# Performance work log

Hardware: AMD Instinct MI355X
Metric: run time of the kernel (lower is better)

Reference implementation:

```python
import jax, jax.numpy as jnp
import numpy as np

N = 100000        # nodes
E = 3200000       # edges (avg degree 32)
D_IN, D_H, D_OUT = 128, 128, 64
EPS = 1e-5        # BatchNorm eps


def setup_inputs() -> dict:
    key = jax.random.key(0)
    ks = jax.random.split(key, 12)
    s = 0.1
    return {
        "x": jax.random.normal(ks[0], (N, D_IN), jnp.float32),
        "edge_index": jax.random.randint(ks[1], (2, E), 0, N, jnp.int32),
        "W1": jax.random.normal(ks[2], (D_IN, D_H), jnp.float32) * s,
        "b1": jnp.zeros((D_H,), jnp.float32),
        "W2": jax.random.normal(ks[3], (D_H, D_H), jnp.float32) * s,
        "b2": jnp.zeros((D_H,), jnp.float32),
        "W3": jax.random.normal(ks[4], (D_H, D_OUT), jnp.float32) * s,
        "b3": jnp.zeros((D_OUT,), jnp.float32),
        "g1": jnp.ones((D_H,), jnp.float32),
        "be1": jnp.zeros((D_H,), jnp.float32),
        "g2": jnp.ones((D_H,), jnp.float32),
        "be2": jnp.zeros((D_H,), jnp.float32),
    }


def reference(x, edge_index, W1, b1, W2, b2, W3, b3, g1, be1, g2, be2):
    # GCNConv normalization: add self-loops, symmetric deg^-1/2 A deg^-1/2
    loop = jnp.arange(N, dtype=edge_index.dtype)
    src = jnp.concatenate([edge_index[0], loop])   # [E+N]
    dst = jnp.concatenate([edge_index[1], loop])   # [E+N]
    deg = jax.ops.segment_sum(jnp.ones(src.shape, x.dtype), dst, num_segments=N)
    dinv = jnp.where(deg > 0, jax.lax.rsqrt(deg), 0.0)
    norm = (dinv[src] * dinv[dst])[:, None]        # [E+N, 1]

    def conv(h, W, b):
        h = h @ W                                   # dense transform [N, d]
        msg = h[src] * norm                         # gather + scale [E+N, d]
        return jax.ops.segment_sum(msg, dst, num_segments=N) + b

    def bn(h, g, be):  # BatchNorm1d over nodes (batch stats, eval-style dropout)
        m = h.mean(axis=0)
        v = h.var(axis=0)
        return (h - m) * jax.lax.rsqrt(v + EPS) * g + be

    h = jax.nn.relu(bn(conv(x, W1, b1), g1, be1))
    h = jax.nn.relu(bn(conv(h, W2, b2), g2, be2))
    h = conv(h, W3, b3)
    return jax.nn.softmax(h, axis=1)
```

## Files before the change

### kernel.cpp

```cpp
#include <hip/hip_runtime.h>
#include <hip/hip_fp16.h>

constexpr int   NN   = 100000;
constexpr int   NE   = 3200000;
constexpr float BN_EPS = 1e-5f;

constexpr int MG_B  = (NN / 32 + 3) / 4;
constexpr int CNT_B = NE / 256;
constexpr int SC_B  = NN * 128 / 4 / 256;

typedef _Float16 half8 __attribute__((ext_vector_type(8)));
typedef float    floatx16 __attribute__((ext_vector_type(16)));

__global__ __launch_bounds__(256) void k_wprep_all(const float* __restrict__ W1,
                                                   const float* __restrict__ W2,
                                                   const float* __restrict__ W3,
                                                   _Float16* __restrict__ Wt1,
                                                   _Float16* __restrict__ Wt2,
                                                   _Float16* __restrict__ Wt3) {
  int idx = blockIdx.x * 256 + threadIdx.x;
  if (idx < 16384) {
    int k = idx >> 7, n = idx & 127;
    Wt1[n * 128 + k] = (_Float16)W1[idx];
  } else if (idx < 32768) {
    int j = idx - 16384, k = j >> 7, n = j & 127;
    Wt2[n * 128 + k] = (_Float16)W2[j];
  } else if (idx < 40960) {
    int j = idx - 32768, k = j >> 6, n = j & 63;
    Wt3[n * 128 + k] = (_Float16)W3[j];
  }
}

__global__ __launch_bounds__(256) void k_f1(const int* __restrict__ dst,
                                            int* __restrict__ deg,
                                            int* __restrict__ slot,
                                            const float* __restrict__ x,
                                            const _Float16* __restrict__ Wt1,
                                            _Float16* __restrict__ C) {
  if (blockIdx.x < MG_B) {
    int wid  = (blockIdx.x * 256 + threadIdx.x) >> 6;
    int lane = threadIdx.x & 63;
    if (wid >= NN / 32) return;
    const int m = lane & 31;
    const int q = lane >> 5;
    const int row0 = wid * 32;
    const float* Arow = x + (size_t)(row0 + m) * 128 + q * 8;

    floatx16 acc[4] = {};
#pragma unroll
    for (int s = 0; s < 8; ++s) {
      float4 a0 = *(const float4*)(Arow + 16 * s);
      float4 a1 = *(const float4*)(Arow + 16 * s + 4);
      half8 af;
      af[0] = (_Float16)a0.x; af[1] = (_Float16)a0.y;
      af[2] = (_Float16)a0.z; af[3] = (_Float16)a0.w;
      af[4] = (_Float16)a1.x; af[5] = (_Float16)a1.y;
      af[6] = (_Float16)a1.z; af[7] = (_Float16)a1.w;
#pragma unroll
      for (int ct = 0; ct < 4; ++ct) {
        half8 bf = *(const half8*)(Wt1 + (size_t)(ct * 32 + m) * 128 + q * 8 + 16 * s);
        acc[ct] = __builtin_amdgcn_mfma_f32_32x32x16_f16(af, bf, acc[ct], 0, 0, 0);
      }
    }
#pragma unroll
    for (int ct = 0; ct < 4; ++ct)
#pragma unroll
      for (int r = 0; r < 16; ++r) {
        int row = (r & 3) + 8 * (r >> 2) + 4 * q;
        C[(size_t)(row0 + row) * 128 + ct * 32 + m] = (_Float16)acc[ct][r];
      }
  } else {
    int e = (blockIdx.x - MG_B) * 256 + threadIdx.x;
    if (e < NE) slot[e] = atomicAdd(&deg[dst[e]], 1);
  }
}

__global__ __launch_bounds__(256) void k_scan_a(const int* __restrict__ deg,
                                                float* __restrict__ dinv,
                                                int* __restrict__ rowptr,
                                                int* __restrict__ bsum) {
  __shared__ int sd[256];
  int t = threadIdx.x;
  int i = blockIdx.x * 256 + t;
  int v = (i < NN) ? deg[i] : 0;
  if (i < NN) dinv[i] = rsqrtf((float)(v + 1));
  sd[t] = v;
  __syncthreads();
  for (int off = 1; off < 256; off <<= 1) {
    int x = (t >= off) ? sd[t - off] : 0;
    __syncthreads();
    sd[t] += x;
    __syncthreads();
  }
  if (i < NN) rowptr[i] = sd[t] - v;
  if (t == 255) bsum[blockIdx.x] = sd[255];
}

__global__ __launch_bounds__(512) void k_scan_b(int* __restrict__ bsum, int nb) {
  __shared__ int sd[512];
  int t = threadIdx.x;
  int v = (t < nb) ? bsum[t] : 0;
  sd[t] = v;
  __syncthreads();
  for (int off = 1; off < 512; off <<= 1) {
    int x = (t >= off) ? sd[t - off] : 0;
    __syncthreads();
    sd[t] += x;
    __syncthreads();
  }
  if (t < nb) bsum[t] = sd[t] - v;
}

__global__ __launch_bounds__(256) void k_scan_c(int* __restrict__ rowptr,
                                                const int* __restrict__ bsum) {
  int i = blockIdx.x * 256 + threadIdx.x;
  if (i < NN) rowptr[i] += bsum[blockIdx.x];
  if (i == 0) rowptr[NN] = NE;
}

__global__ __launch_bounds__(256) void k_f2(const int* __restrict__ ei,
                                            const int* __restrict__ rowptr,
                                            const int* __restrict__ slot,
                                            int* __restrict__ csrc,
                                            const float* __restrict__ dinv,
                                            uint2* __restrict__ Hf) {
  if (blockIdx.x < SC_B) {
    int i = blockIdx.x * 256 + threadIdx.x;
    int row = i >> 5;
    float dv = dinv[row];
    uint2 v = Hf[i];
    __half2 h0 = *(__half2*)&v.x;
    __half2 h1 = *(__half2*)&v.y;
    float2 f0 = __half22float2(h0);
    float2 f1 = __half22float2(h1);
    h0 = __floats2half2_rn(f0.x * dv, f0.y * dv);
    h1 = __floats2half2_rn(f1.x * dv, f1.y * dv);
    v.x = *(unsigned*)&h0;
    v.y = *(unsigned*)&h1;
    Hf[i] = v;
  } else {
    int e = (blockIdx.x - SC_B) * 256 + threadIdx.x;
    if (e >= NE) return;
    int s = ei[e];
    int d = ei[NE + e];
    csrc[rowptr[d] + slot[e]] = s;
  }
}

template <int BN_>
__global__ __launch_bounds__(256) void k_mgemm(const _Float16* __restrict__ A,
                                               const _Float16* __restrict__ Wt,
                                               const float* __restrict__ scale,
                                               const float* __restrict__ shift,
                                               const float* __restrict__ dinv,
                                               _Float16* __restrict__ C) {
  constexpr int NCT = BN_ / 32;
  int wid  = (blockIdx.x * 256 + threadIdx.x) >> 6;
  int lane = threadIdx.x & 63;
  if (wid >= NN / 32) return;
  const int m = lane & 31;
  const int q = lane >> 5;
  const int row0 = wid * 32;

  const _Float16* Arow = A + (size_t)(row0 + m) * 128 + q * 8;

  floatx16 acc[NCT] = {};

#pragma unroll
  for (int s = 0; s < 8; ++s) {
    half8 raw = *(const half8*)(Arow + 16 * s);
    int k0 = 16 * s + q * 8;
    half8 af;
#pragma unroll
    for (int j = 0; j < 8; ++j) {
      float a = fmaxf(fmaf((float)raw[j], scale[k0 + j], shift[k0 + j]), 0.f);
      af[j] = (_Float16)a;
    }
#pragma unroll
    for (int ct = 0; ct < NCT; ++ct) {
      half8 bf = *(const half8*)(Wt + (size_t)(ct * 32 + m) * 128 + q * 8 + 16 * s);
      acc[ct] = __builtin_amdgcn_mfma_f32_32x32x16_f16(af, bf, acc[ct], 0, 0, 0);
    }
  }

#pragma unroll
  for (int ct = 0; ct < NCT; ++ct)
#pragma unroll
    for (int r = 0; r < 16; ++r) {
      int row = (r & 3) + 8 * (r >> 2) + 4 * q;
      float dv = dinv[row0 + row];
      C[(size_t)(row0 + row) * BN_ + ct * 32 + m] = (_Float16)(acc[ct][r] * dv);
    }
}

__global__ __launch_bounds__(256) void k_agg128(const __half* __restrict__ H,
                                                const float* __restrict__ dinv,
                                                const int* __restrict__ rowptr,
                                                const int* __restrict__ srcs,
                                                __half2* __restrict__ out) {
  int wid  = (blockIdx.x * 256 + threadIdx.x) >> 6;
  int lane = threadIdx.x & 63;
  if (wid >= NN) return;
  const __half2* Hp = (const __half2*)H;
  float2 acc = __half22float2(Hp[(size_t)wid * 64 + lane]);
  int beg = rowptr[wid], end = rowptr[wid + 1];
  int e = beg;
  int end8 = beg + ((end - beg) & ~7);
  for (; e < end8; e += 8) {
    __half2 v0 = Hp[(size_t)srcs[e+0] * 64 + lane];
    __half2 v1 = Hp[(size_t)srcs[e+1] * 64 + lane];
    __half2 v2 = Hp[(size_t)srcs[e+2] * 64 + lane];
    __half2 v3 = Hp[(size_t)srcs[e+3] * 64 + lane];
    __half2 v4 = Hp[(size_t)srcs[e+4] * 64 + lane];
    __half2 v5 = Hp[(size_t)srcs[e+5] * 64 + lane];
    __half2 v6 = Hp[(size_t)srcs[e+6] * 64 + lane];
    __half2 v7 = Hp[(size_t)srcs[e+7] * 64 + lane];
    float2 f0 = __half22float2(v0), f1 = __half22float2(v1);
    float2 f2 = __half22float2(v2), f3 = __half22float2(v3);
    float2 f4 = __half22float2(v4), f5 = __half22float2(v5);
    float2 f6 = __half22float2(v6), f7 = __half22float2(v7);
    acc.x += (f0.x + f1.x) + (f2.x + f3.x) + (f4.x + f5.x) + (f6.x + f7.x);
    acc.y += (f0.y + f1.y) + (f2.y + f3.y) + (f4.y + f5.y) + (f6.y + f7.y);
  }
  for (; e < end; ++e) {
    float2 f = __half22float2(Hp[(size_t)srcs[e] * 64 + lane]);
    acc.x += f.x; acc.y += f.y;
  }
  float di = dinv[wid];
  out[(size_t)wid * 64 + lane] = __floats2half2_rn(acc.x * di, acc.y * di);
}

__global__ __launch_bounds__(256) void k_agg64_softmax(const __half* __restrict__ H,
                                                       const float* __restrict__ dinv,
                                                       const int* __restrict__ rowptr,
                                                       const int* __restrict__ srcs,
                                                       const float* __restrict__ b3,
                                                       float* __restrict__ out) {
  int wid  = (blockIdx.x * 256 + threadIdx.x) >> 6;
  int lane = threadIdx.x & 63;
  if (wid >= NN) return;
  float acc = __half2float(H[(size_t)wid * 64 + lane]);
  int beg = rowptr[wid], end = rowptr[wid + 1];
  int e = beg;
  int end8 = beg + ((end - beg) & ~7);
  for (; e < end8; e += 8) {
    float v0 = __half2float(H[(size_t)srcs[e+0] * 64 + lane]);
    float v1 = __half2float(H[(size_t)srcs[e+1] * 64 + lane]);
    float v2 = __half2float(H[(size_t)srcs[e+2] * 64 + lane]);
    float v3 = __half2float(H[(size_t)srcs[e+3] * 64 + lane]);
    float v4 = __half2float(H[(size_t)srcs[e+4] * 64 + lane]);
    float v5 = __half2float(H[(size_t)srcs[e+5] * 64 + lane]);
    float v6 = __half2float(H[(size_t)srcs[e+6] * 64 + lane]);
    float v7 = __half2float(H[(size_t)srcs[e+7] * 64 + lane]);
    acc += (v0 + v1) + (v2 + v3) + (v4 + v5) + (v6 + v7);
  }
  for (; e < end; ++e)
    acc += __half2float(H[(size_t)srcs[e] * 64 + lane]);
  acc = acc * dinv[wid] + b3[lane];

  float m = acc;
#pragma unroll
  for (int off = 32; off > 0; off >>= 1) m = fmaxf(m, __shfl_xor(m, off));
  float ev = __expf(acc - m);
  float s = ev;
#pragma unroll
  for (int off = 32; off > 0; off >>= 1) s += __shfl_xor(s, off);
  out[(size_t)wid * 64 + lane] = ev / s;
}

__global__ __launch_bounds__(256) void k_stats(const __half2* __restrict__ H2,
                                               float* __restrict__ S1,
                                               float* __restrict__ S2) {
  int t = threadIdx.x;
  int p = t & 63;
  int r = t >> 6;
  float2 s1 = {0.f, 0.f}, s2 = {0.f, 0.f};
  for (int row = blockIdx.x * 4 + r; row < NN; row += gridDim.x * 4) {
    float2 v = __half22float2(H2[(size_t)row * 64 + p]);
    s1.x += v.x; s1.y += v.y;
    s2.x += v.x * v.x; s2.y += v.y * v.y;
  }
  __shared__ float2 l1[256], l2[256];
  l1[t] = s1; l2[t] = s2;
  __syncthreads();
  if (t < 128) {
    l1[t].x += l1[t+128].x; l1[t].y += l1[t+128].y;
    l2[t].x += l2[t+128].x; l2[t].y += l2[t+128].y;
  }
  __syncthreads();
  if (t < 64) {
    float2 a1 = l1[t], b1 = l1[t+64];
    float2 a2 = l2[t], b2 = l2[t+64];
    atomicAdd(&S1[2*p+0], a1.x + b1.x);
    atomicAdd(&S1[2*p+1], a1.y + b1.y);
    atomicAdd(&S2[2*p+0], a2.x + b2.x);
    atomicAdd(&S2[2*p+1], a2.y + b2.y);
  }
}

__global__ void k_finalize(const float* __restrict__ S1, const float* __restrict__ S2,
                           const float* __restrict__ g,  const float* __restrict__ be,
                           float* __restrict__ scale,    float* __restrict__ shift) {
  int t = threadIdx.x;
  float mean = S1[t] * (1.0f / NN);
  float var  = S2[t] * (1.0f / NN) - mean * mean;
  float is   = rsqrtf(var + BN_EPS);
  float sc   = g[t] * is;
  scale[t] = sc;
  shift[t] = be[t] - mean * sc;
}

extern "C" void kernel_launch(void* const* d_in, const int* in_sizes, int n_in,
                              void* d_out, int out_size, void* d_ws, size_t ws_size,
                              hipStream_t stream) {
  (void)in_sizes; (void)n_in; (void)out_size; (void)ws_size;
  const float* x   = (const float*)d_in[0];
  const int*   ei  = (const int*)d_in[1];
  const float* W1  = (const float*)d_in[2];
  const float* W2  = (const float*)d_in[4];
  const float* W3  = (const float*)d_in[6];
  const float* b3  = (const float*)d_in[7];
  const float* g1  = (const float*)d_in[8];
  const float* be1 = (const float*)d_in[9];
  const float* g2  = (const float*)d_in[10];
  const float* be2 = (const float*)d_in[11];
  float* out = (float*)d_out;

  char* ws = (char*)d_ws;
  size_t off = 0;
  auto take = [&](size_t bytes) -> char* {
    char* p = ws + off;
    off = (off + bytes + 255) & ~(size_t)255;
    return p;
  };
  int*   deg    = (int*)  take((size_t)NN * 4);
  float* S1a    = (float*)take(128 * 4);
  float* S2a    = (float*)take(128 * 4);
  float* S1b    = (float*)take(128 * 4);
  float* S2b    = (float*)take(128 * 4);
  size_t zero_bytes = off;
  float* scale1 = (float*)take(128 * 4);
  float* shift1 = (float*)take(128 * 4);
  float* scale2 = (float*)take(128 * 4);
  float* shift2 = (float*)take(128 * 4);
  float* dinv   = (float*)take((size_t)NN * 4);
  int*   rowptr = (int*)  take((size_t)(NN + 1) * 4);
  int*   bsum   = (int*)  take(1024 * 4);
  int*   slot   = (int*)  take((size_t)NE * 4);
  int*   csrc   = (int*)  take((size_t)NE * 4);
  _Float16* Wt1 = (_Float16*)take((size_t)128 * 128 * 2);
  _Float16* Wt2 = (_Float16*)take((size_t)128 * 128 * 2);
  _Float16* Wt3 = (_Float16*)take((size_t)64 * 128 * 2);
  _Float16* Hf  = (_Float16*)take((size_t)NN * 128 * 2);
  _Float16* hB  = (_Float16*)take((size_t)NN * 128 * 2);

  (void)hipMemsetAsync(d_ws, 0, zero_bytes, stream);

  const int nbN  = (NN + 255) / 256;
  const int mgB  = MG_B;
  const int aggB = (NN + 3) / 4;

  k_wprep_all<<<160, 256, 0, stream>>>(W1, W2, W3, Wt1, Wt2, Wt3);

  k_f1<<<MG_B + CNT_B, 256, 0, stream>>>(ei + NE, deg, slot, x, Wt1, Hf);

  k_scan_a<<<nbN, 256, 0, stream>>>(deg, dinv, rowptr, bsum);
  k_scan_b<<<1, 512, 0, stream>>>(bsum, nbN);
  k_scan_c<<<nbN, 256, 0, stream>>>(rowptr, bsum);

  k_f2<<<SC_B + CNT_B, 256, 0, stream>>>(ei, rowptr, slot, csrc, dinv, (uint2*)Hf);

  k_agg128<<<aggB, 256, 0, stream>>>((const __half*)Hf, dinv, rowptr, csrc, (__half2*)hB);
  k_stats<<<1024, 256, 0, stream>>>((const __half2*)hB, S1a, S2a);
  k_finalize<<<1, 128, 0, stream>>>(S1a, S2a, g1, be1, scale1, shift1);

  k_mgemm<128><<<mgB, 256, 0, stream>>>(hB, Wt2, scale1, shift1, dinv, Hf);
  k_agg128<<<aggB, 256, 0, stream>>>((const __half*)Hf, dinv, rowptr, csrc, (__half2*)hB);
  k_stats<<<1024, 256, 0, stream>>>((const __half2*)hB, S1b, S2b);
  k_finalize<<<1, 128, 0, stream>>>(S1b, S2b, g2, be2, scale2, shift2);

  k_mgemm<64><<<mgB, 256, 0, stream>>>(hB, Wt3, scale2, shift2, dinv, Hf);
  k_agg64_softmax<<<aggB, 256, 0, stream>>>((const __half*)Hf, dinv, rowptr, csrc, b3, out);
}
```

Baseline: 840.5 us.

## Build CSR via two-level bucket sort instead of global atomic degree counting

Replaces the global-atomic degree count plus slot-based scatter with a two-level counting sort. Per-chunk shared-memory histograms over 128-node buckets are scanned, edges are scattered into buckets, then each bucket is locally sorted by node to produce rowptr, dinv and csrc. This removes contended global atomics and the random csrc writes. The separate pre-scaling of the first-layer features by dinv is dropped; the first aggregation instead applies source-node dinv inline, which adds per-edge dinv gathers to that pass. Node ids are packed into 17 bits and the local offset into the upper bits, which holds for N=100000.

```diff
diff --git a/kernel.cpp b/kernel.cpp
--- a/kernel.cpp
+++ b/kernel.cpp
@@ -6,8 +6,9 @@
 constexpr float BN_EPS = 1e-5f;
 
 constexpr int MG_B  = (NN / 32 + 3) / 4;
-constexpr int CNT_B = NE / 256;
-constexpr int SC_B  = NN * 128 / 4 / 256;
+constexpr int NB    = (NN + 127) / 128;
+constexpr int HB    = 256;
+constexpr int CHUNK = NE / HB;
 
 typedef _Float16 half8 __attribute__((ext_vector_type(8)));
 typedef float    floatx16 __attribute__((ext_vector_type(16)));
@@ -32,11 +33,11 @@
 }
 
 __global__ __launch_bounds__(256) void k_f1(const int* __restrict__ dst,
-                                            int* __restrict__ deg,
-                                            int* __restrict__ slot,
+                                            int* __restrict__ blkhist,
                                             const float* __restrict__ x,
                                             const _Float16* __restrict__ Wt1,
                                             _Float16* __restrict__ C) {
+  __shared__ int h[NB];
   if (blockIdx.x < MG_B) {
     int wid  = (blockIdx.x * 256 + threadIdx.x) >> 6;
     int lane = threadIdx.x & 63;
@@ -70,80 +71,121 @@
         C[(size_t)(row0 + row) * 128 + ct * 32 + m] = (_Float16)acc[ct][r];
       }
   } else {
-    int e = (blockIdx.x - MG_B) * 256 + threadIdx.x;
-    if (e < NE) slot[e] = atomicAdd(&deg[dst[e]], 1);
-  }
-}
-
-__global__ __launch_bounds__(256) void k_scan_a(const int* __restrict__ deg,
-                                                float* __restrict__ dinv,
-                                                int* __restrict__ rowptr,
-                                                int* __restrict__ bsum) {
-  __shared__ int sd[256];
+    int j = blockIdx.x - MG_B;
+    int t = threadIdx.x;
+    for (int b = t; b < NB; b += 256) h[b] = 0;
+    __syncthreads();
+    int base = j * CHUNK;
+    for (int e = base + t; e < base + CHUNK; e += 256)
+      atomicAdd(&h[dst[e] >> 7], 1);
+    __syncthreads();
+    for (int b = t; b < NB; b += 256) blkhist[j * NB + b] = h[b];
+  }
+}
+
+__global__ __launch_bounds__(256) void k_scan_bkt_a(const int* __restrict__ blkhist,
+                                                    int* __restrict__ blkbase,
+                                                    int* __restrict__ total) {
+  int wid  = (blockIdx.x * 256 + threadIdx.x) >> 6;
+  int lane = threadIdx.x & 63;
+  if (wid >= NB) return;
+  int i0 = lane * 4;
+  int v0 = blkhist[(i0 + 0) * NB + wid];
+  int v1 = blkhist[(i0 + 1) * NB + wid];
+  int v2 = blkhist[(i0 + 2) * NB + wid];
+  int v3 = blkhist[(i0 + 3) * NB + wid];
+  int lt = v0 + v1 + v2 + v3;
+  int inc = lt;
+#pragma unroll
+  for (int off = 1; off < 64; off <<= 1) {
+    int xx = __shfl_up(inc, off);
+    if (lane >= off) inc += xx;
+  }
+  int exc = inc - lt;
+  blkbase[(i0 + 0) * NB + wid] = exc;
+  blkbase[(i0 + 1) * NB + wid] = exc + v0;
+  blkbase[(i0 + 2) * NB + wid] = exc + v0 + v1;
+  blkbase[(i0 + 3) * NB + wid] = exc + v0 + v1 + v2;
+  if (lane == 63) total[wid] = inc;
+}
+
+__global__ __launch_bounds__(1024) void k_scan_bkt_b(const int* __restrict__ total,
+                                                     int* __restrict__ bbase) {
+  __shared__ int s[1024];
   int t = threadIdx.x;
-  int i = blockIdx.x * 256 + t;
-  int v = (i < NN) ? deg[i] : 0;
-  if (i < NN) dinv[i] = rsqrtf((float)(v + 1));
-  sd[t] = v;
-  __syncthreads();
-  for (int off = 1; off < 256; off <<= 1) {
-    int x = (t >= off) ? sd[t - off] : 0;
-    __syncthreads();
-    sd[t] += x;
-    __syncthreads();
-  }
-  if (i < NN) rowptr[i] = sd[t] - v;
-  if (t == 255) bsum[blockIdx.x] = sd[255];
-}
-
-__global__ __launch_bounds__(512) void k_scan_b(int* __restrict__ bsum, int nb) {
-  __shared__ int sd[512];
+  int v = (t < NB) ? total[t] : 0;
+  s[t] = v;
+  __syncthreads();
+  for (int off = 1; off < 1024; off <<= 1) {
+    int xx = (t >= off) ? s[t - off] : 0;
+    __syncthreads();
+    s[t] += xx;
+    __syncthreads();
+  }
+  if (t < NB) bbase[t] = s[t] - v;
+  if (t == NB - 1) bbase[NB] = s[t];
+}
+
+__global__ __launch_bounds__(256) void k_scatter(const int* __restrict__ ei,
+                                                 const int* __restrict__ bbase,
+                                                 const int* __restrict__ blkbase,
+                                                 int* __restrict__ ebuf) {
+  __shared__ int cur[NB];
+  int i = blockIdx.x;
   int t = threadIdx.x;
-  int v = (t < nb) ? bsum[t] : 0;
-  sd[t] = v;
-  __syncthreads();
-  for (int off = 1; off < 512; off <<= 1) {
-    int x = (t >= off) ? sd[t - off] : 0;
-    __syncthreads();
-    sd[t] += x;
-    __syncthreads();
-  }
-  if (t < nb) bsum[t] = sd[t] - v;
-}
-
-__global__ __launch_bounds__(256) void k_scan_c(int* __restrict__ rowptr,
-                                                const int* __restrict__ bsum) {
-  int i = blockIdx.x * 256 + threadIdx.x;
-  if (i < NN) rowptr[i] += bsum[blockIdx.x];
-  if (i == 0) rowptr[NN] = NE;
-}
-
-__global__ __launch_bounds__(256) void k_f2(const int* __restrict__ ei,
-                                            const int* __restrict__ rowptr,
-                                            const int* __restrict__ slot,
-                                            int* __restrict__ csrc,
-                                            const float* __restrict__ dinv,
-                                            uint2* __restrict__ Hf) {
-  if (blockIdx.x < SC_B) {
-    int i = blockIdx.x * 256 + threadIdx.x;
-    int row = i >> 5;
-    float dv = dinv[row];
-    uint2 v = Hf[i];
-    __half2 h0 = *(__half2*)&v.x;
-    __half2 h1 = *(__half2*)&v.y;
-    float2 f0 = __half22float2(h0);
-    float2 f1 = __half22float2(h1);
-    h0 = __floats2half2_rn(f0.x * dv, f0.y * dv);
-    h1 = __floats2half2_rn(f1.x * dv, f1.y * dv);
-    v.x = *(unsigned*)&h0;
-    v.y = *(unsigned*)&h1;
-    Hf[i] = v;
-  } else {
-    int e = (blockIdx.x - SC_B) * 256 + threadIdx.x;
-    if (e >= NE) return;
+  for (int b = t; b < NB; b += 256) cur[b] = bbase[b] + blkbase[i * NB + b];
+  __syncthreads();
+  int base = i * CHUNK;
+  for (int e = base + t; e < base + CHUNK; e += 256) {
     int s = ei[e];
     int d = ei[NE + e];
-    csrc[rowptr[d] + slot[e]] = s;
+    int b = d >> 7;
+    int pos = atomicAdd(&cur[b], 1);
+    ebuf[pos] = s | ((d & 127) << 17);
+  }
+}
+
+__global__ __launch_bounds__(256) void k_bucket(const int* __restrict__ bbase,
+                                                const int* __restrict__ ebuf,
+                                                int* __restrict__ rowptr,
+                                                float* __restrict__ dinv,
+                                                int* __restrict__ csrc) {
+  __shared__ int degL[128];
+  __shared__ int sc[128];
+  __shared__ int curL[128];
+  int b = blockIdx.x;
+  int t = threadIdx.x;
+  int e0 = bbase[b], e1 = bbase[b + 1];
+  if (t < 128) degL[t] = 0;
+  __syncthreads();
+  for (int e = e0 + t; e < e1; e += 256)
+    atomicAdd(&degL[ebuf[e] >> 17], 1);
+  __syncthreads();
+  if (t < 128) sc[t] = degL[t];
+  __syncthreads();
+  for (int off = 1; off < 128; off <<= 1) {
+    int xx = 0;
+    if (t < 128 && t >= off) xx = sc[t - off];
+    __syncthreads();
+    if (t < 128) sc[t] += xx;
+    __syncthreads();
+  }
+  if (t < 128) {
+    int node = b * 128 + t;
+    if (node < NN) {
+      int d = degL[t];
+      int exc = sc[t] - d;
+      rowptr[node] = e0 + exc;
+      dinv[node] = rsqrtf((float)(d + 1));
+      curL[t] = exc;
+    }
+  }
+  if (b == NB - 1 && t == 0) rowptr[NN] = NE;
+  __syncthreads();
+  for (int e = e0 + t; e < e1; e += 256) {
+    int p = ebuf[e];
+    int pos = atomicAdd(&curL[p >> 17], 1);
+    csrc[e0 + pos] = p & 0x1FFFF;
   }
 }
 
@@ -193,6 +235,7 @@
     }
 }
 
+template <bool SRCSCALE>
 __global__ __launch_bounds__(256) void k_agg128(const __half* __restrict__ H,
                                                 const float* __restrict__ dinv,
                                                 const int* __restrict__ rowptr,
@@ -202,31 +245,55 @@
   int lane = threadIdx.x & 63;
   if (wid >= NN) return;
   const __half2* Hp = (const __half2*)H;
-  float2 acc = __half22float2(Hp[(size_t)wid * 64 + lane]);
+  float di = dinv[wid];
+  float2 self = __half22float2(Hp[(size_t)wid * 64 + lane]);
+  float2 acc;
+  if (SRCSCALE) { acc.x = self.x * di; acc.y = self.y * di; }
+  else          { acc = self; }
   int beg = rowptr[wid], end = rowptr[wid + 1];
   int e = beg;
   int end8 = beg + ((end - beg) & ~7);
   for (; e < end8; e += 8) {
-    __half2 v0 = Hp[(size_t)srcs[e+0] * 64 + lane];
-    __half2 v1 = Hp[(size_t)srcs[e+1] * 64 + lane];
-    __half2 v2 = Hp[(size_t)srcs[e+2] * 64 + lane];
-    __half2 v3 = Hp[(size_t)srcs[e+3] * 64 + lane];
-    __half2 v4 = Hp[(size_t)srcs[e+4] * 64 + lane];
-    __half2 v5 = Hp[(size_t)srcs[e+5] * 64 + lane];
-    __half2 v6 = Hp[(size_t)srcs[e+6] * 64 + lane];
-    __half2 v7 = Hp[(size_t)srcs[e+7] * 64 + lane];
+    int s0 = srcs[e+0], s1 = srcs[e+1], s2 = srcs[e+2], s3 = srcs[e+3];
+    int s4 = srcs[e+4], s5 = srcs[e+5], s6 = srcs[e+6], s7 = srcs[e+7];
+    __half2 v0 = Hp[(size_t)s0 * 64 + lane];
+    __half2 v1 = Hp[(size_t)s1 * 64 + lane];
+    __half2 v2 = Hp[(size_t)s2 * 64 + lane];
+    __half2 v3 = Hp[(size_t)s3 * 64 + lane];
+    __half2 v4 = Hp[(size_t)s4 * 64 + lane];
+    __half2 v5 = Hp[(size_t)s5 * 64 + lane];
+    __half2 v6 = Hp[(size_t)s6 * 64 + lane];
+    __half2 v7 = Hp[(size_t)s7 * 64 + lane];
     float2 f0 = __half22float2(v0), f1 = __half22float2(v1);
     float2 f2 = __half22float2(v2), f3 = __half22float2(v3);
     float2 f4 = __half22float2(v4), f5 = __half22float2(v5);
     float2 f6 = __half22float2(v6), f7 = __half22float2(v7);
-    acc.x += (f0.x + f1.x) + (f2.x + f3.x) + (f4.x + f5.x) + (f6.x + f7.x);
-    acc.y += (f0.y + f1.y) + (f2.y + f3.y) + (f4.y + f5.y) + (f6.y + f7.y);
+    if (SRCSCALE) {
+      float d0 = dinv[s0], d1 = dinv[s1], d2 = dinv[s2], d3 = dinv[s3];
+      float d4 = dinv[s4], d5 = dinv[s5], d6 = dinv[s6], d7 = dinv[s7];
+      acc.x = fmaf(f0.x, d0, acc.x); acc.y = fmaf(f0.y, d0, acc.y);
+      acc.x = fmaf(f1.x, d1, acc.x); acc.y = fmaf(f1.y, d1, acc.y);
+      acc.x = fmaf(f2.x, d2, acc.x); acc.y = fmaf(f2.y, d2, acc.y);
+      acc.x = fmaf(f3.x, d3, acc.x); acc.y = fmaf(f3.y, d3, acc.y);
+      acc.x = fmaf(f4.x, d4, acc.x); acc.y = fmaf(f4.y, d4, acc.y);
+      acc.x = fmaf(f5.x, d5, acc.x); acc.y = fmaf(f5.y, d5, acc.y);
+      acc.x = fmaf(f6.x, d6, acc.x); acc.y = fmaf(f6.y, d6, acc.y);
+      acc.x = fmaf(f7.x, d7, acc.x); acc.y = fmaf(f7.y, d7, acc.y);
+    } else {
+      acc.x += (f0.x + f1.x) + (f2.x + f3.x) + (f4.x + f5.x) + (f6.x + f7.x);
+      acc.y += (f0.y + f1.y) + (f2.y + f3.y) + (f4.y + f5.y) + (f6.y + f7.y);
+    }
   }
   for (; e < end; ++e) {
-    float2 f = __half22float2(Hp[(size_t)srcs[e] * 64 + lane]);
-    acc.x += f.x; acc.y += f.y;
-  }
-  float di = dinv[wid];
+    int s = srcs[e];
+    float2 f = __half22float2(Hp[(size_t)s * 64 + lane]);
+    if (SRCSCALE) {
+      float dd = dinv[s];
+      acc.x = fmaf(f.x, dd, acc.x); acc.y = fmaf(f.y, dd, acc.y);
+    } else {
+      acc.x += f.x; acc.y += f.y;
+    }
+  }
   out[(size_t)wid * 64 + lane] = __floats2half2_rn(acc.x * di, acc.y * di);
 }
 
@@ -333,7 +400,6 @@
     off = (off + bytes + 255) & ~(size_t)255;
     return p;
   };
-  int*   deg    = (int*)  take((size_t)NN * 4);
   float* S1a    = (float*)take(128 * 4);
   float* S2a    = (float*)take(128 * 4);
   float* S1b    = (float*)take(128 * 4);
@@ -345,8 +411,11 @@
   float* shift2 = (float*)take(128 * 4);
   float* dinv   = (float*)take((size_t)NN * 4);
   int*   rowptr = (int*)  take((size_t)(NN + 1) * 4);
-  int*   bsum   = (int*)  take(1024 * 4);
-  int*   slot   = (int*)  take((size_t)NE * 4);
+  int*   bbase  = (int*)  take((size_t)(NB + 1) * 4);
+  int*   total  = (int*)  take((size_t)NB * 4);
+  int*   blkhist= (int*)  take((size_t)HB * NB * 4);
+  int*   blkbase= (int*)  take((size_t)HB * NB * 4);
+  int*   ebuf   = (int*)  take((size_t)NE * 4);
   int*   csrc   = (int*)  take((size_t)NE * 4);
   _Float16* Wt1 = (_Float16*)take((size_t)128 * 128 * 2);
   _Float16* Wt2 = (_Float16*)take((size_t)128 * 128 * 2);
@@ -356,26 +425,25 @@
 
   (void)hipMemsetAsync(d_ws, 0, zero_bytes, stream);
 
-  const int nbN  = (NN + 255) / 256;
   const int mgB  = MG_B;
   const int aggB = (NN + 3) / 4;
+  const int scanAB = (NB + 3) / 4;
 
   k_wprep_all<<<160, 256, 0, stream>>>(W1, W2, W3, Wt1, Wt2, Wt3);
 
-  k_f1<<<MG_B + CNT_B, 256, 0, stream>>>(ei + NE, deg, slot, x, Wt1, Hf);
-
-  k_scan_a<<<nbN, 256, 0, stream>>>(deg, dinv, rowptr, bsum);
-  k_scan_b<<<1, 512, 0, stream>>>(bsum, nbN);
-  k_scan_c<<<nbN, 256, 0, stream>>>(rowptr, bsum);
-
-  k_f2<<<SC_B + CNT_B, 256, 0, stream>>>(ei, rowptr, slot, csrc, dinv, (uint2*)Hf);
-
-  k_agg128<<<aggB, 256, 0, stream>>>((const __half*)Hf, dinv, rowptr, csrc, (__half2*)hB);
+  k_f1<<<MG_B + HB, 256, 0, stream>>>(ei + NE, blkhist, x, Wt1, Hf);
+
+  k_scan_bkt_a<<<scanAB, 256, 0, stream>>>(blkhist, blkbase, total);
+  k_scan_bkt_b<<<1, 1024, 0, stream>>>(total, bbase);
+  k_scatter<<<HB, 256, 0, stream>>>(ei, bbase, blkbase, ebuf);
+  k_bucket<<<NB, 256, 0, stream>>>(bbase, ebuf, rowptr, dinv, csrc);
+
+  k_agg128<true><<<aggB, 256, 0, stream>>>((const __half*)Hf, dinv, rowptr, csrc, (__half2*)hB);
   k_stats<<<1024, 256, 0, stream>>>((const __half2*)hB, S1a, S2a);
   k_finalize<<<1, 128, 0, stream>>>(S1a, S2a, g1, be1, scale1, shift1);
 
   k_mgemm<128><<<mgB, 256, 0, stream>>>(hB, Wt2, scale1, shift1, dinv, Hf);
-  k_agg128<<<aggB, 256, 0, stream>>>((const __half*)Hf, dinv, rowptr, csrc, (__half2*)hB);
+  k_agg128<false><<<aggB, 256, 0, stream>>>((const __half*)Hf, dinv, rowptr, csrc, (__half2*)hB);
   k_stats<<<1024, 256, 0, stream>>>((const __half2*)hB, S1b, S2b);
   k_finalize<<<1, 128, 0, stream>>>(S1b, S2b, g2, be2, scale2, shift2);
 
```

New measurement: 732.4 us. -12.9%, faster.
